# Optimization experiments

Measured on AMD Instinct MI355X. Metric: run time of the kernel, lower is better.

Reference implementation:

```python
import jax, jax.numpy as jnp
import numpy as np

N_HEADS = 16
SCALE = 8.0  # sqrt(inner_dim // n_heads) = sqrt(64), scale='inv_sqrt'


def setup_inputs() -> dict:
    key = jax.random.key(0)
    k1, k2, k3, k4 = jax.random.split(key, 4)
    b, n, d_model, inner = 8, 2048, 1024, 1024
    x = jax.random.normal(k1, (b, n, d_model), dtype=jnp.float32)
    Wqkv = jax.random.normal(k2, (3 * inner, d_model), dtype=jnp.float32) * (1.0 / np.sqrt(d_model))
    Wproj = jax.random.normal(k3, (d_model, inner), dtype=jnp.float32) * (1.0 / np.sqrt(inner))
    bproj = jax.random.normal(k4, (d_model,), dtype=jnp.float32) * 0.01
    return {"x": x, "Wqkv": Wqkv, "Wproj": Wproj, "bproj": bproj}


def reference(x, Wqkv, Wproj, bproj):
    b, n, _ = x.shape
    qkv = jnp.einsum('bnm,fm->bnf', x, Wqkv)          # [b, n, 3*inner]
    qkv = qkv.reshape(b, n, N_HEADS, -1)              # [b, n, h, 3*dh] (einops 'b n (h d)')
    dh = qkv.shape[3] // 3
    q, k, v = qkv[..., :dh], qkv[..., dh:2 * dh], qkv[..., 2 * dh:]
    # Faithful to source: q @ k.transpose(-1,-2) on [b,n,h,dh] -> scores over HEADS, [b,n,h,h]
    scores = jnp.einsum('bnhd,bngd->bnhg', q, k) / SCALE
    attn = jax.nn.softmax(scores, axis=-1)            # softmax over last head axis
    out = jnp.einsum('bnhg,bngd->bnhd', attn, v)      # [b, n, h, dh]
    out = out.reshape(b, n, -1)                       # [b, n, inner]
    return jnp.einsum('bni,mi->bnm', out, Wproj) + bproj
```

## Files before the change

### kernel.cpp

```cpp
#include <hip/hip_runtime.h>
#include <stdint.h>

typedef __bf16 bf16_t;
typedef __bf16 bf16x8 __attribute__((ext_vector_type(8)));
typedef float f32x4 __attribute__((ext_vector_type(4)));

__device__ __forceinline__ void gload_lds16(const void* g, void* l) {
  __builtin_amdgcn_global_load_lds(
      (const __attribute__((address_space(1))) uint32_t*)g,
      (__attribute__((address_space(3))) uint32_t*)l, 16, 0, 0);
}

__global__ void cast3_f32_bf16(const float* __restrict__ a, bf16_t* __restrict__ ao, int n4a,
                               const float* __restrict__ b, bf16_t* __restrict__ bo, int n4b,
                               const float* __restrict__ c, bf16_t* __restrict__ co, int n4c) {
  int i = blockIdx.x * blockDim.x + threadIdx.x;
  int stride = gridDim.x * blockDim.x;
  int total = n4a + n4b + n4c;
  for (int idx = i; idx < total; idx += stride) {
    const float* src; bf16_t* dst; int j = idx;
    if (j < n4a) { src = a; dst = ao; }
    else if ((j -= n4a) < n4b) { src = b; dst = bo; }
    else { j -= n4b; src = c; dst = co; }
    float4 v = reinterpret_cast<const float4*>(src)[j];
    union { bf16_t b[4]; uint2 u; } pk;
    pk.b[0] = (bf16_t)v.x; pk.b[1] = (bf16_t)v.y;
    pk.b[2] = (bf16_t)v.z; pk.b[3] = (bf16_t)v.w;
    reinterpret_cast<uint2*>(dst)[j] = pk.u;
  }
}

template <bool BF16_OUT>
__global__ __launch_bounds__(512, 2)
void gemm_pipe(const bf16_t* __restrict__ A, const bf16_t* __restrict__ B,
               void* __restrict__ Cout, const float* __restrict__ bias,
               int N) {
  constexpr int K = 1024, NT = 32;
  __shared__ bf16_t Al[4][256 * 32];
  __shared__ bf16_t Bl[4][256 * 32];

  const int tid = threadIdx.x;
  const int l = tid & 63, w = tid >> 6;
  const int wm = w >> 2, wn = w & 3;

  const int bid = blockIdx.x;
  const int xcd = bid & 7;
  const int idx = bid >> 3;
  const int bx = xcd * 8 + (idx & 7);
  const int by = idx >> 3;
  const int m0 = bx * 256, n0 = by * 256;

  const int ra = tid >> 2;
  const int ca = ((tid & 3) ^ ((tid >> 3) & 3)) * 8;
  const bf16_t* pA0 = A + (size_t)(m0 +   0 + ra) * K + ca;
  const bf16_t* pA1 = A + (size_t)(m0 + 128 + ra) * K + ca;
  const bf16_t* pB0 = B + (size_t)(n0 +   0 + ra) * K + ca;
  const bf16_t* pB1 = B + (size_t)(n0 + 128 + ra) * K + ca;
  const int wb = w * 512;

#define STAGE(t_, s_) do {                          \
    const int kt_ = (t_) * 32;                      \
    gload_lds16(pA0 + kt_, &Al[s_][wb]);            \
    gload_lds16(pA1 + kt_, &Al[s_][4096 + wb]);     \
    gload_lds16(pB0 + kt_, &Bl[s_][wb]);            \
    gload_lds16(pB1 + kt_, &Bl[s_][4096 + wb]);     \
  } while (0)

  const int abase = (wm * 128 + (l & 15)) * 32;
  const int bbase = (wn * 64 + (l & 15)) * 32;
  const int ck = ((l >> 4) ^ ((l >> 1) & 3)) * 8;

  f32x4 acc[8][4] = {};

  STAGE(0, 0);
  STAGE(1, 1);
  STAGE(2, 2);

  int slot = 0;
  for (int t = 0; t < NT; ++t) {
    if (t < NT - 2)       asm volatile("s_waitcnt vmcnt(8)" ::: "memory");
    else if (t == NT - 2) asm volatile("s_waitcnt vmcnt(4)" ::: "memory");
    else                  asm volatile("s_waitcnt vmcnt(0)" ::: "memory");
    __builtin_amdgcn_s_barrier();
    asm volatile("" ::: "memory");
    if (t + 3 < NT) {
      int s3 = (slot + 3) & 3;
      STAGE(t + 3, s3);
    }
    const bf16_t* As = Al[slot];
    const bf16_t* Bs = Bl[slot];
    bf16x8 af[8], bfr[4];
#pragma unroll
    for (int i = 0; i < 8; ++i)
      af[i] = *reinterpret_cast<const bf16x8*>(&As[abase + i * 512 + ck]);
#pragma unroll
    for (int j = 0; j < 4; ++j)
      bfr[j] = *reinterpret_cast<const bf16x8*>(&Bs[bbase + j * 512 + ck]);
    __builtin_amdgcn_s_setprio(1);
#pragma unroll
    for (int i = 0; i < 8; ++i)
#pragma unroll
      for (int j = 0; j < 4; ++j)
        acc[i][j] = __builtin_amdgcn_mfma_f32_16x16x32_bf16(af[i], bfr[j],
                                                            acc[i][j], 0, 0, 0);
    __builtin_amdgcn_s_setprio(0);
    slot = (slot + 1) & 3;
  }
#undef STAGE

  const int r0 = m0 + wm * 128 + (l >> 4) * 4;
  const int c0 = n0 + wn * 64 + (l & 15);
  if (BF16_OUT) {
    bf16_t* C = (bf16_t*)Cout;
#pragma unroll
    for (int i = 0; i < 8; ++i)
#pragma unroll
      for (int j = 0; j < 4; ++j)
#pragma unroll
        for (int r = 0; r < 4; ++r)
          C[(size_t)(r0 + i * 16 + r) * N + (c0 + j * 16)] = (bf16_t)acc[i][j][r];
  } else {
    float* C = (float*)Cout;
#pragma unroll
    for (int i = 0; i < 8; ++i)
#pragma unroll
      for (int j = 0; j < 4; ++j)
#pragma unroll
        for (int r = 0; r < 4; ++r)
          C[(size_t)(r0 + i * 16 + r) * N + (c0 + j * 16)] =
              acc[i][j][r] + bias[c0 + j * 16];
  }
}

__global__ __launch_bounds__(256)
void attn_heads(const bf16_t* __restrict__ qkv, bf16_t* __restrict__ out) {
  __shared__ float s[4][3072];
  const int w = threadIdx.x >> 6, l = threadIdx.x & 63;
  const size_t t = (size_t)blockIdx.x * 4 + w;
  const bf16_t* src = qkv + t * 3072;
#pragma unroll
  for (int i = 0; i < 6; ++i) {
    int f = (i * 64 + l) * 8;
    bf16x8 v = *reinterpret_cast<const bf16x8*>(&src[f]);
#pragma unroll
    for (int jj = 0; jj < 8; ++jj) s[w][f + jj] = (float)v[jj];
  }
  __syncthreads();

  const int h = l >> 2, ss = l & 3;
  float qr[16];
  const float* qb = &s[w][h * 192 + ss * 16];
#pragma unroll
  for (int d = 0; d < 16; ++d) qr[d] = qb[d];

  float sc[16];
#pragma unroll
  for (int g = 0; g < 16; ++g) {
    const float* kk = &s[w][g * 192 + 64 + ss * 16];
    float p = 0.f;
#pragma unroll
    for (int d = 0; d < 16; ++d) p += qr[d] * kk[d];
    p += __shfl_xor(p, 1);
    p += __shfl_xor(p, 2);
    sc[g] = p * 0.125f;
  }
  float m = sc[0];
#pragma unroll
  for (int g = 1; g < 16; ++g) m = fmaxf(m, sc[g]);
  float sum = 0.f;
#pragma unroll
  for (int g = 0; g < 16; ++g) { sc[g] = __expf(sc[g] - m); sum += sc[g]; }
  float inv = 1.f / sum;

  float o[16] = {};
#pragma unroll
  for (int g = 0; g < 16; ++g) {
    float a = sc[g] * inv;
    const float* vv = &s[w][g * 192 + 128 + ss * 16];
#pragma unroll
    for (int d = 0; d < 16; ++d) o[d] += a * vv[d];
  }
  union { bf16_t b[16]; uint4 u[2]; } pk;
#pragma unroll
  for (int d = 0; d < 16; ++d) pk.b[d] = (bf16_t)o[d];
  uint4* dst = reinterpret_cast<uint4*>(out + t * 1024 + h * 64 + ss * 16);
  dst[0] = pk.u[0];
  dst[1] = pk.u[1];
}

extern "C" void kernel_launch(void* const* d_in, const int* in_sizes, int n_in,
                              void* d_out, int out_size, void* d_ws, size_t ws_size,
                              hipStream_t stream) {
  const float* x     = (const float*)d_in[0];
  const float* Wqkv  = (const float*)d_in[1];
  const float* Wproj = (const float*)d_in[2];
  const float* bproj = (const float*)d_in[3];
  float* out = (float*)d_out;

  const int M = 8 * 2048;
  const int DM = 1024;
  const int F = 3072;

  char* ws = (char*)d_ws;
  bf16_t* xb     = (bf16_t*)ws;  ws += (size_t)M * DM * 2;
  bf16_t* wqkvb  = (bf16_t*)ws;  ws += (size_t)F * DM * 2;
  bf16_t* wprojb = (bf16_t*)ws;  ws += (size_t)DM * DM * 2;
  bf16_t* qkvb   = (bf16_t*)ws;  ws += (size_t)M * F * 2;
  bf16_t* attnb  = (bf16_t*)ws;

  cast3_f32_bf16<<<2048, 256, 0, stream>>>(x, xb, M * DM / 4,
                                           Wqkv, wqkvb, F * DM / 4,
                                           Wproj, wprojb, DM * DM / 4);

  gemm_pipe<true><<<(M / 256) * (F / 256), 512, 0, stream>>>(
      xb, wqkvb, (void*)qkvb, nullptr, F);

  attn_heads<<<M / 4, 256, 0, stream>>>(qkvb, attnb);

  gemm_pipe<false><<<(M / 256) * (DM / 256), 512, 0, stream>>>(
      attnb, wprojb, (void*)out, bproj, DM);
}
```

Baseline: 238.6 us.

## Split GEMM main loop into two half-phases interleaving LDS reads, prefetch and MFMA

Restructures the GEMM K-loop into two phases per tile. Each phase loads half of the A fragments from LDS, issues half of the global-to-LDS prefetch for a future stage, synchronises with barriers, then runs 16 MFMAs. The aim is to spread memory issue across the loop and overlap LDS reads and global loads with matrix work, in the style of ping-pong scheduling. In exchange it adds more barriers per iteration, and the vmcnt wait bookkeeping becomes more fragile.

```diff
diff --git a/kernel.cpp b/kernel.cpp
--- a/kernel.cpp
+++ b/kernel.cpp
@@ -58,13 +58,12 @@
   const bf16_t* pB1 = B + (size_t)(n0 + 128 + ra) * K + ca;
   const int wb = w * 512;
 
-#define STAGE(t_, s_) do {                          \
-    const int kt_ = (t_) * 32;                      \
-    gload_lds16(pA0 + kt_, &Al[s_][wb]);            \
-    gload_lds16(pA1 + kt_, &Al[s_][4096 + wb]);     \
-    gload_lds16(pB0 + kt_, &Bl[s_][wb]);            \
-    gload_lds16(pB1 + kt_, &Bl[s_][4096 + wb]);     \
-  } while (0)
+#define STAGE_A(t_, s_) do { const int kt_ = (t_) * 32;          \
+    gload_lds16(pA0 + kt_, &Al[s_][wb]);                         \
+    gload_lds16(pA1 + kt_, &Al[s_][4096 + wb]); } while (0)
+#define STAGE_B(t_, s_) do { const int kt_ = (t_) * 32;          \
+    gload_lds16(pB0 + kt_, &Bl[s_][wb]);                         \
+    gload_lds16(pB1 + kt_, &Bl[s_][4096 + wb]); } while (0)
 
   const int abase = (wm * 128 + (l & 15)) * 32;
   const int bbase = (wn * 64 + (l & 15)) * 32;
@@ -72,41 +71,61 @@
 
   f32x4 acc[8][4] = {};
 
-  STAGE(0, 0);
-  STAGE(1, 1);
-  STAGE(2, 2);
-
-  int slot = 0;
+  STAGE_A(0, 0); STAGE_B(0, 0);
+  STAGE_A(1, 1); STAGE_B(1, 1);
+  STAGE_A(2, 2); STAGE_B(2, 2);
+  asm volatile("s_waitcnt vmcnt(8)" ::: "memory");
+  __builtin_amdgcn_s_barrier();
+
   for (int t = 0; t < NT; ++t) {
-    if (t < NT - 2)       asm volatile("s_waitcnt vmcnt(8)" ::: "memory");
-    else if (t == NT - 2) asm volatile("s_waitcnt vmcnt(4)" ::: "memory");
-    else                  asm volatile("s_waitcnt vmcnt(0)" ::: "memory");
-    __builtin_amdgcn_s_barrier();
-    asm volatile("" ::: "memory");
-    if (t + 3 < NT) {
-      int s3 = (slot + 3) & 3;
-      STAGE(t + 3, s3);
-    }
+    const int slot = t & 3;
+    const int s3 = (t + 3) & 3;
     const bf16_t* As = Al[slot];
     const bf16_t* Bs = Bl[slot];
-    bf16x8 af[8], bfr[4];
-#pragma unroll
-    for (int i = 0; i < 8; ++i)
-      af[i] = *reinterpret_cast<const bf16x8*>(&As[abase + i * 512 + ck]);
+    bf16x8 af0[4], af1[4], bfr[4];
+
+#pragma unroll
+    for (int i = 0; i < 4; ++i)
+      af0[i] = *reinterpret_cast<const bf16x8*>(&As[abase + i * 512 + ck]);
 #pragma unroll
     for (int j = 0; j < 4; ++j)
       bfr[j] = *reinterpret_cast<const bf16x8*>(&Bs[bbase + j * 512 + ck]);
+    if (t + 3 < NT) STAGE_A(t + 3, s3);
+    __builtin_amdgcn_s_barrier();
+    asm volatile("s_waitcnt lgkmcnt(0)" ::: "memory");
+    __builtin_amdgcn_sched_barrier(0);
     __builtin_amdgcn_s_setprio(1);
 #pragma unroll
-    for (int i = 0; i < 8; ++i)
-#pragma unroll
-      for (int j = 0; j < 4; ++j)
-        acc[i][j] = __builtin_amdgcn_mfma_f32_16x16x32_bf16(af[i], bfr[j],
+    for (int i = 0; i < 4; ++i)
+#pragma unroll
+      for (int j = 0; j < 4; ++j)
+        acc[i][j] = __builtin_amdgcn_mfma_f32_16x16x32_bf16(af0[i], bfr[j],
                                                             acc[i][j], 0, 0, 0);
     __builtin_amdgcn_s_setprio(0);
-    slot = (slot + 1) & 3;
-  }
-#undef STAGE
+    __builtin_amdgcn_s_barrier();
+
+#pragma unroll
+    for (int i = 0; i < 4; ++i)
+      af1[i] = *reinterpret_cast<const bf16x8*>(&As[abase + (i + 4) * 512 + ck]);
+    if (t + 3 < NT) STAGE_B(t + 3, s3);
+    __builtin_amdgcn_s_barrier();
+    asm volatile("s_waitcnt lgkmcnt(0)" ::: "memory");
+    __builtin_amdgcn_sched_barrier(0);
+    __builtin_amdgcn_s_setprio(1);
+#pragma unroll
+    for (int i = 0; i < 4; ++i)
+#pragma unroll
+      for (int j = 0; j < 4; ++j)
+        acc[i + 4][j] = __builtin_amdgcn_mfma_f32_16x16x32_bf16(af1[i], bfr[j],
+                                                                acc[i + 4][j], 0, 0, 0);
+    __builtin_amdgcn_s_setprio(0);
+    if (t + 3 < NT)       asm volatile("s_waitcnt vmcnt(8)" ::: "memory");
+    else if (t == NT - 3) asm volatile("s_waitcnt vmcnt(4)" ::: "memory");
+    else if (t == NT - 2) asm volatile("s_waitcnt vmcnt(0)" ::: "memory");
+    __builtin_amdgcn_s_barrier();
+  }
+#undef STAGE_A
+#undef STAGE_B
 
   const int r0 = m0 + wm * 128 + (l >> 4) * 4;
   const int c0 = n0 + wn * 64 + (l & 15);
```

Result: faster. 214.9 us (-9.9%).

## Restructure GEMM into 8-phase ping-pong schedule with BK=64 half-tile loads

Applied to the files above, without the earlier changes.

Replaces the 4-stage BK=32 GEMM pipeline with a double-buffered BK=64 scheme. A and B are split into 128-row halves, and each K-step is cut into four sub-phases that interleave LDS fragment reads, global-to-LDS loads and MFMA quarter-blocks, separated by barriers. The aim is to overlap memory traffic with matrix-core work at finer granularity, with fewer K iterations and a wider XOR swizzle. It adds many barriers and hand-tuned waitcnt counts, which risks stalls or races if the counts are wrong.

```diff
diff --git a/kernel.cpp b/kernel.cpp
--- a/kernel.cpp
+++ b/kernel.cpp
@@ -32,81 +32,133 @@
 
 template <bool BF16_OUT>
 __global__ __launch_bounds__(512, 2)
-void gemm_pipe(const bf16_t* __restrict__ A, const bf16_t* __restrict__ B,
-               void* __restrict__ Cout, const float* __restrict__ bias,
-               int N) {
-  constexpr int K = 1024, NT = 32;
-  __shared__ bf16_t Al[4][256 * 32];
-  __shared__ bf16_t Bl[4][256 * 32];
+void gemm_8ph(const bf16_t* __restrict__ A, const bf16_t* __restrict__ B,
+              void* __restrict__ Cout, const float* __restrict__ bias, int N) {
+  constexpr int K = 1024, NI = 8;
+  __shared__ bf16_t Al[2][2][128 * 64];
+  __shared__ bf16_t Bl[2][2][128 * 64];
 
   const int tid = threadIdx.x;
   const int l = tid & 63, w = tid >> 6;
   const int wm = w >> 2, wn = w & 3;
 
   const int bid = blockIdx.x;
-  const int xcd = bid & 7;
-  const int idx = bid >> 3;
+  const int xcd = bid & 7, idx = bid >> 3;
   const int bx = xcd * 8 + (idx & 7);
   const int by = idx >> 3;
   const int m0 = bx * 256, n0 = by * 256;
 
-  const int ra = tid >> 2;
-  const int ca = ((tid & 3) ^ ((tid >> 3) & 3)) * 8;
-  const bf16_t* pA0 = A + (size_t)(m0 +   0 + ra) * K + ca;
-  const bf16_t* pA1 = A + (size_t)(m0 + 128 + ra) * K + ca;
-  const bf16_t* pB0 = B + (size_t)(n0 +   0 + ra) * K + ca;
-  const bf16_t* pB1 = B + (size_t)(n0 + 128 + ra) * K + ca;
-  const int wb = w * 512;
-
-#define STAGE(t_, s_) do {                          \
-    const int kt_ = (t_) * 32;                      \
-    gload_lds16(pA0 + kt_, &Al[s_][wb]);            \
-    gload_lds16(pA1 + kt_, &Al[s_][4096 + wb]);     \
-    gload_lds16(pB0 + kt_, &Bl[s_][wb]);            \
-    gload_lds16(pB1 + kt_, &Bl[s_][4096 + wb]);     \
-  } while (0)
-
-  const int abase = (wm * 128 + (l & 15)) * 32;
-  const int bbase = (wn * 64 + (l & 15)) * 32;
-  const int ck = ((l >> 4) ^ ((l >> 1) & 3)) * 8;
+  const int srow = tid >> 3;
+  const int sca = ((tid & 7) ^ (srow & 7)) * 8;
+  const bf16_t* pA = A + (size_t)(m0 + srow) * K + sca;
+  const bf16_t* pB = B + (size_t)(n0 + srow) * K + sca;
+
+#define ST_A(t_, d_, h_) do {                                                         \
+    gload_lds16(pA + (size_t)((h_) * 128) * K + (t_) * 64, &Al[d_][h_][tid * 8]);     \
+    gload_lds16(pA + (size_t)((h_) * 128 + 64) * K + (t_) * 64,                       \
+                &Al[d_][h_][4096 + tid * 8]); } while (0)
+#define ST_B(t_, d_, h_) do {                                                         \
+    gload_lds16(pB + (size_t)((h_) * 128) * K + (t_) * 64, &Bl[d_][h_][tid * 8]);     \
+    gload_lds16(pB + (size_t)((h_) * 128 + 64) * K + (t_) * 64,                       \
+                &Bl[d_][h_][4096 + tid * 8]); } while (0)
+
+  const int arow = l & 15;
+  const int brow = (wn & 1) * 64 + (l & 15);
+  const int cks0 = (((l >> 4) + 0) ^ (l & 7)) * 8;
+  const int cks1 = (((l >> 4) + 4) ^ (l & 7)) * 8;
+
+#define LDA4(dst, base, i0) do {                                                      \
+    _Pragma("unroll") for (int i = 0; i < 4; ++i) {                                   \
+      dst[i][0] = *reinterpret_cast<const bf16x8*>(&base[(arow + (i0 + i) * 16) * 64 + cks0]); \
+      dst[i][1] = *reinterpret_cast<const bf16x8*>(&base[(arow + (i0 + i) * 16) * 64 + cks1]); \
+    } } while (0)
+#define LDB2(dst, base, j0) do {                                                      \
+    _Pragma("unroll") for (int j = 0; j < 2; ++j) {                                   \
+      dst[j][0] = *reinterpret_cast<const bf16x8*>(&base[(brow + (j0 + j) * 16) * 64 + cks0]); \
+      dst[j][1] = *reinterpret_cast<const bf16x8*>(&base[(brow + (j0 + j) * 16) * 64 + cks1]); \
+    } } while (0)
+
+#define MM16(afr, bfr, I0, J0)                                                        \
+    __builtin_amdgcn_s_setprio(1);                                                    \
+    _Pragma("unroll") for (int i = 0; i < 4; ++i)                                     \
+    _Pragma("unroll") for (int j = 0; j < 2; ++j)                                     \
+    _Pragma("unroll") for (int s = 0; s < 2; ++s)                                     \
+      acc[I0 + i][J0 + j] = __builtin_amdgcn_mfma_f32_16x16x32_bf16(                  \
+          afr[i][s], bfr[j][s], acc[I0 + i][J0 + j], 0, 0, 0);                        \
+    __builtin_amdgcn_s_setprio(0);
+
+#define BAR()    __builtin_amdgcn_s_barrier()
+#define LGKM0()  do { asm volatile("s_waitcnt lgkmcnt(0)" ::: "memory");              \
+                      __builtin_amdgcn_sched_barrier(0); } while (0)
 
   f32x4 acc[8][4] = {};
 
-  STAGE(0, 0);
-  STAGE(1, 1);
-  STAGE(2, 2);
-
-  int slot = 0;
-  for (int t = 0; t < NT; ++t) {
-    if (t < NT - 2)       asm volatile("s_waitcnt vmcnt(8)" ::: "memory");
-    else if (t == NT - 2) asm volatile("s_waitcnt vmcnt(4)" ::: "memory");
-    else                  asm volatile("s_waitcnt vmcnt(0)" ::: "memory");
-    __builtin_amdgcn_s_barrier();
-    asm volatile("" ::: "memory");
-    if (t + 3 < NT) {
-      int s3 = (slot + 3) & 3;
-      STAGE(t + 3, s3);
-    }
-    const bf16_t* As = Al[slot];
-    const bf16_t* Bs = Bl[slot];
-    bf16x8 af[8], bfr[4];
-#pragma unroll
-    for (int i = 0; i < 8; ++i)
-      af[i] = *reinterpret_cast<const bf16x8*>(&As[abase + i * 512 + ck]);
-#pragma unroll
-    for (int j = 0; j < 4; ++j)
-      bfr[j] = *reinterpret_cast<const bf16x8*>(&Bs[bbase + j * 512 + ck]);
-    __builtin_amdgcn_s_setprio(1);
-#pragma unroll
-    for (int i = 0; i < 8; ++i)
-#pragma unroll
-      for (int j = 0; j < 4; ++j)
-        acc[i][j] = __builtin_amdgcn_mfma_f32_16x16x32_bf16(af[i], bfr[j],
-                                                            acc[i][j], 0, 0, 0);
-    __builtin_amdgcn_s_setprio(0);
-    slot = (slot + 1) & 3;
-  }
-#undef STAGE
+  ST_A(0, 0, 0); ST_A(0, 0, 1); ST_B(0, 0, 0); ST_B(0, 0, 1);
+  ST_B(1, 1, 0); ST_B(1, 1, 1);
+  asm volatile("s_waitcnt vmcnt(4)" ::: "memory");
+  BAR();
+
+  for (int it = 0; it < NI; ++it) {
+    const bool last = (it == NI - 1);
+    const int ta = 2 * it, tb = ta + 1;
+    const bf16_t* As0 = &Al[0][wm][0];
+    const bf16_t* Bs0 = &Bl[0][wn >> 1][0];
+    const bf16_t* As1 = &Al[1][wm][0];
+    const bf16_t* Bs1 = &Bl[1][wn >> 1][0];
+    bf16x8 af0[4][2], af1[4][2], bf0[2][2], bf1[2][2];
+
+    LDA4(af0, As0, 0); LDB2(bf0, Bs0, 0);
+    ST_A(tb, 1, 0);
+    asm volatile("s_waitcnt lgkmcnt(8)" ::: "memory");
+    BAR(); LGKM0();
+    MM16(af0, bf0, 0, 0);
+    BAR();
+    LDB2(bf1, Bs0, 2);
+    ST_A(tb, 1, 1);
+    BAR(); LGKM0();
+    MM16(af0, bf1, 0, 2);
+    BAR();
+    LDA4(af1, As0, 4);
+    if (!last) ST_B(ta + 2, 0, 0);
+    BAR(); LGKM0();
+    MM16(af1, bf0, 4, 0);
+    BAR();
+    if (!last) ST_B(ta + 2, 0, 1);
+    BAR();
+    MM16(af1, bf1, 4, 2);
+    if (last) asm volatile("s_waitcnt vmcnt(0)" ::: "memory");
+    else      asm volatile("s_waitcnt vmcnt(2)" ::: "memory");
+    BAR();
+
+    LDA4(af0, As1, 0); LDB2(bf0, Bs1, 0);
+    if (!last) ST_A(ta + 2, 0, 0);
+    asm volatile("s_waitcnt lgkmcnt(8)" ::: "memory");
+    BAR(); LGKM0();
+    MM16(af0, bf0, 0, 0);
+    BAR();
+    LDB2(bf1, Bs1, 2);
+    if (!last) ST_A(ta + 2, 0, 1);
+    BAR(); LGKM0();
+    MM16(af0, bf1, 0, 2);
+    BAR();
+    LDA4(af1, As1, 4);
+    if (!last) ST_B(tb + 2, 1, 0);
+    BAR(); LGKM0();
+    MM16(af1, bf0, 4, 0);
+    BAR();
+    if (!last) ST_B(tb + 2, 1, 1);
+    BAR();
+    MM16(af1, bf1, 4, 2);
+    if (!last) asm volatile("s_waitcnt vmcnt(2)" ::: "memory");
+    BAR();
+  }
+#undef ST_A
+#undef ST_B
+#undef LDA4
+#undef LDB2
+#undef MM16
+#undef BAR
+#undef LGKM0
 
   const int r0 = m0 + wm * 128 + (l >> 4) * 4;
   const int c0 = n0 + wn * 64 + (l & 15);
@@ -212,11 +264,11 @@
                                            Wqkv, wqkvb, F * DM / 4,
                                            Wproj, wprojb, DM * DM / 4);
 
-  gemm_pipe<true><<<(M / 256) * (F / 256), 512, 0, stream>>>(
+  gemm_8ph<true><<<(M / 256) * (F / 256), 512, 0, stream>>>(
       xb, wqkvb, (void*)qkvb, nullptr, F);
 
   attn_heads<<<M / 4, 256, 0, stream>>>(qkvb, attnb);
 
-  gemm_pipe<false><<<(M / 256) * (DM / 256), 512, 0, stream>>>(
+  gemm_8ph<false><<<(M / 256) * (DM / 256), 512, 0, stream>>>(
       attnb, wprojb, (void*)out, bproj, DM);
 }
```

After: 200.8 us. 15.8% less time.

## Software-pipeline LDS fragment reads with MFMA in GEMM main loop

Applied to the files above, without the earlier changes.

Restructures the GEMM k-loop so LDS fragment reads run ahead of the MFMAs that use them. The next tile's low A and B fragments are loaded while the current tile's second half computes, and the A upper half is read in the middle of the tile. Double-buffered register fragments and fine-grained lgkmcnt waits replace the single read-then-compute phase, with one barrier per tile moved to the end. This aims to hide LDS latency behind MFMA issue, at the cost of more registers and subtle wait-count correctness.

```diff
diff --git a/kernel.cpp b/kernel.cpp
--- a/kernel.cpp
+++ b/kernel.cpp
@@ -32,9 +32,8 @@
 
 template <bool BF16_OUT>
 __global__ __launch_bounds__(512, 2)
-void gemm_pipe(const bf16_t* __restrict__ A, const bf16_t* __restrict__ B,
-               void* __restrict__ Cout, const float* __restrict__ bias,
-               int N) {
+void gemm_rp(const bf16_t* __restrict__ A, const bf16_t* __restrict__ B,
+             void* __restrict__ Cout, const float* __restrict__ bias, int N) {
   constexpr int K = 1024, NT = 32;
   __shared__ bf16_t Al[4][256 * 32];
   __shared__ bf16_t Bl[4][256 * 32];
@@ -44,69 +43,88 @@
   const int wm = w >> 2, wn = w & 3;
 
   const int bid = blockIdx.x;
-  const int xcd = bid & 7;
-  const int idx = bid >> 3;
+  const int xcd = bid & 7, idx = bid >> 3;
   const int bx = xcd * 8 + (idx & 7);
   const int by = idx >> 3;
   const int m0 = bx * 256, n0 = by * 256;
 
   const int ra = tid >> 2;
   const int ca = ((tid & 3) ^ ((tid >> 3) & 3)) * 8;
-  const bf16_t* pA0 = A + (size_t)(m0 +   0 + ra) * K + ca;
+  const bf16_t* pA0 = A + (size_t)(m0 + ra) * K + ca;
   const bf16_t* pA1 = A + (size_t)(m0 + 128 + ra) * K + ca;
-  const bf16_t* pB0 = B + (size_t)(n0 +   0 + ra) * K + ca;
+  const bf16_t* pB0 = B + (size_t)(n0 + ra) * K + ca;
   const bf16_t* pB1 = B + (size_t)(n0 + 128 + ra) * K + ca;
   const int wb = w * 512;
 
-#define STAGE(t_, s_) do {                          \
-    const int kt_ = (t_) * 32;                      \
-    gload_lds16(pA0 + kt_, &Al[s_][wb]);            \
-    gload_lds16(pA1 + kt_, &Al[s_][4096 + wb]);     \
-    gload_lds16(pB0 + kt_, &Bl[s_][wb]);            \
-    gload_lds16(pB1 + kt_, &Bl[s_][4096 + wb]);     \
-  } while (0)
+#define STAGE(t_, s_) do { const int kt_ = (t_) * 32;  \
+    gload_lds16(pA0 + kt_, &Al[s_][wb]);               \
+    gload_lds16(pA1 + kt_, &Al[s_][4096 + wb]);        \
+    gload_lds16(pB0 + kt_, &Bl[s_][wb]);               \
+    gload_lds16(pB1 + kt_, &Bl[s_][4096 + wb]); } while (0)
 
   const int abase = (wm * 128 + (l & 15)) * 32;
   const int bbase = (wn * 64 + (l & 15)) * 32;
   const int ck = ((l >> 4) ^ ((l >> 1) & 3)) * 8;
 
   f32x4 acc[8][4] = {};
-
-  STAGE(0, 0);
-  STAGE(1, 1);
-  STAGE(2, 2);
-
-  int slot = 0;
-  for (int t = 0; t < NT; ++t) {
-    if (t < NT - 2)       asm volatile("s_waitcnt vmcnt(8)" ::: "memory");
-    else if (t == NT - 2) asm volatile("s_waitcnt vmcnt(4)" ::: "memory");
-    else                  asm volatile("s_waitcnt vmcnt(0)" ::: "memory");
-    __builtin_amdgcn_s_barrier();
-    asm volatile("" ::: "memory");
-    if (t + 3 < NT) {
-      int s3 = (slot + 3) & 3;
-      STAGE(t + 3, s3);
-    }
-    const bf16_t* As = Al[slot];
-    const bf16_t* Bs = Bl[slot];
-    bf16x8 af[8], bfr[4];
-#pragma unroll
-    for (int i = 0; i < 8; ++i)
-      af[i] = *reinterpret_cast<const bf16x8*>(&As[abase + i * 512 + ck]);
-#pragma unroll
-    for (int j = 0; j < 4; ++j)
-      bfr[j] = *reinterpret_cast<const bf16x8*>(&Bs[bbase + j * 512 + ck]);
-    __builtin_amdgcn_s_setprio(1);
-#pragma unroll
-    for (int i = 0; i < 8; ++i)
-#pragma unroll
-      for (int j = 0; j < 4; ++j)
-        acc[i][j] = __builtin_amdgcn_mfma_f32_16x16x32_bf16(af[i], bfr[j],
-                                                            acc[i][j], 0, 0, 0);
+  bf16x8 afA[4], bfA[4], afB[4], bfB[4], ah[4];
+
+#define RD_LO(af_, bf_, s_) do {                                               \
+    const bf16_t* As_ = Al[s_]; const bf16_t* Bs_ = Bl[s_];                    \
+    _Pragma("unroll") for (int j = 0; j < 4; ++j)                              \
+      bf_[j] = *reinterpret_cast<const bf16x8*>(&Bs_[bbase + j * 512 + ck]);   \
+    _Pragma("unroll") for (int i = 0; i < 4; ++i)                              \
+      af_[i] = *reinterpret_cast<const bf16x8*>(&As_[abase + i * 512 + ck]);   \
+  } while (0)
+#define RD_HI(s_) do { const bf16_t* As_ = Al[s_];                             \
+    _Pragma("unroll") for (int i = 0; i < 4; ++i)                              \
+      ah[i] = *reinterpret_cast<const bf16x8*>(&As_[abase + (i + 4) * 512 + ck]); \
+  } while (0)
+
+#define MM16(af_, bf_, R0)                                                     \
+    __builtin_amdgcn_s_setprio(1);                                             \
+    _Pragma("unroll") for (int i = 0; i < 4; ++i)                              \
+    _Pragma("unroll") for (int j = 0; j < 4; ++j)                              \
+      acc[(R0) + i][j] = __builtin_amdgcn_mfma_f32_16x16x32_bf16(              \
+          af_[i], bf_[j], acc[(R0) + i][j], 0, 0, 0);                          \
     __builtin_amdgcn_s_setprio(0);
-    slot = (slot + 1) & 3;
+
+#define BARF() do { asm volatile("" ::: "memory");  \
+    __builtin_amdgcn_s_barrier();                   \
+    asm volatile("" ::: "memory"); } while (0)
+
+#define TILE(t_, AFc, BFc, AFn, BFn) do {                                 \
+    RD_HI((t_) & 3);                                                      \
+    if ((t_) + 3 < NT) STAGE((t_) + 3, ((t_) + 3) & 3);                   \
+    asm volatile("s_waitcnt lgkmcnt(4)" ::: "memory");                    \
+    MM16(AFc, BFc, 0);                                                    \
+    if ((t_) + 1 < NT) {                                                  \
+      RD_LO(AFn, BFn, ((t_) + 1) & 3);                                    \
+      asm volatile("s_waitcnt lgkmcnt(8)" ::: "memory");                  \
+    } else {                                                              \
+      asm volatile("s_waitcnt lgkmcnt(0)" ::: "memory");                  \
+    }                                                                     \
+    MM16(ah, BFc, 4);                                                     \
+    if ((t_) + 3 < NT) asm volatile("s_waitcnt vmcnt(4)" ::: "memory");   \
+    else               asm volatile("s_waitcnt vmcnt(0)" ::: "memory");   \
+    BARF();                                                               \
+  } while (0)
+
+  STAGE(0, 0); STAGE(1, 1); STAGE(2, 2);
+  asm volatile("s_waitcnt vmcnt(4)" ::: "memory");
+  BARF();
+  RD_LO(afA, bfA, 0);
+
+  for (int tt = 0; tt < NT; tt += 2) {
+    TILE(tt, afA, bfA, afB, bfB);
+    TILE(tt + 1, afB, bfB, afA, bfA);
   }
 #undef STAGE
+#undef RD_LO
+#undef RD_HI
+#undef MM16
+#undef BARF
+#undef TILE
 
   const int r0 = m0 + wm * 128 + (l >> 4) * 4;
   const int c0 = n0 + wn * 64 + (l & 15);
@@ -212,11 +230,11 @@
                                            Wqkv, wqkvb, F * DM / 4,
                                            Wproj, wprojb, DM * DM / 4);
 
-  gemm_pipe<true><<<(M / 256) * (F / 256), 512, 0, stream>>>(
+  gemm_rp<true><<<(M / 256) * (F / 256), 512, 0, stream>>>(
       xb, wqkvb, (void*)qkvb, nullptr, F);
 
   attn_heads<<<M / 4, 256, 0, stream>>>(qkvb, attnb);
 
-  gemm_pipe<false><<<(M / 256) * (DM / 256), 512, 0, stream>>>(
+  gemm_rp<false><<<(M / 256) * (DM / 256), 512, 0, stream>>>(
       attnb, wprojb, (void*)out, bproj, DM);
 }
```

Result: faster. 216.2 us (-9.4%).
